# Optimization experiments

Hardware: AMD Instinct MI355X
Metric: run time of the kernel (lower is better)

## Reference

```python
import jax, jax.numpy as jnp
import numpy as np

B_, N_, D_ = 8, 1024, 64
H_, DH_ = 4, 16
DI_, DS_, DTR_ = 128, 64, 4
MAXP = 512


def _ln(x, w, b, eps=1e-5):
    m = jnp.mean(x, -1, keepdims=True)
    v = jnp.mean((x - m) ** 2, -1, keepdims=True)
    return (x - m) * jax.lax.rsqrt(v + eps) * w + b


def _attn(x, drop_mask, Wq, Wkv, Wo, bo, rel_emb):
    b, n, d = x.shape
    scale = DH_ ** -0.5
    q = (x @ Wq).reshape(b, n, H_, DH_).transpose(0, 2, 1, 3)
    kv = x @ Wkv
    k = kv[..., :d].reshape(b, n, H_, DH_).transpose(0, 2, 1, 3)
    v = kv[..., d:].reshape(b, n, H_, DH_).transpose(0, 2, 1, 3)
    dots = jnp.einsum('bhid,bhjd->bhij', q, k) * scale
    seq = jnp.arange(n)
    dist = jnp.clip(seq[:, None] - seq[None, :], -MAXP, MAXP) + MAXP
    rpe = rel_emb[dist]  # (n, n, DH_)
    dots = dots + jnp.einsum('bhid,ijd->bhij', q, rpe) * scale
    # stochastic key drop: Bernoulli(0.3) positions get -1e12
    dots = dots + drop_mask.astype(dots.dtype) * (-1e12)
    attn = jax.nn.softmax(dots, axis=-1)
    out = jnp.einsum('bhij,bhjd->bhid', attn, v)
    out = out.transpose(0, 2, 1, 3).reshape(b, n, H_ * DH_)
    return out @ Wo + bo


def _mamba(x, W_in, conv_w, conv_b, W_xproj, W_dt, b_dt, A_log, Dm, W_out):
    b, n, _ = x.shape
    xz = x @ W_in                      # (b, n, 2*DI_)
    u, z = xz[..., :DI_], xz[..., DI_:]
    uc = u.transpose(0, 2, 1)          # (b, DI_, n)
    uc = jax.lax.conv_general_dilated(
        uc, conv_w[:, None, :], (1,), ((3, 0),),
        feature_group_count=DI_, dimension_numbers=('NCH', 'OIH', 'NCH'))
    uc = uc + conv_b[None, :, None]
    u = jax.nn.silu(uc).transpose(0, 2, 1)  # (b, n, DI_)
    xdb = u @ W_xproj                  # (b, n, DTR_+2*DS_)
    dt = jax.nn.softplus(xdb[..., :DTR_] @ W_dt + b_dt)  # (b, n, DI_)
    Bm = xdb[..., DTR_:DTR_ + DS_]
    Cm = xdb[..., DTR_ + DS_:]
    A = -jnp.exp(A_log)                # (DI_, DS_)

    def step(h, inp):
        dt_t, B_t, C_t, u_t = inp      # (b,DI_),(b,DS_),(b,DS_),(b,DI_)
        dA = jnp.exp(dt_t[..., None] * A)
        h = h * dA + (dt_t * u_t)[..., None] * B_t[:, None, :]
        y = jnp.einsum('bds,bs->bd', h, C_t)
        return h, y

    h0 = jnp.zeros((b, DI_, DS_), x.dtype)
    xs = (dt.transpose(1, 0, 2), Bm.transpose(1, 0, 2),
          Cm.transpose(1, 0, 2), u.transpose(1, 0, 2))
    _, ys = jax.lax.scan(step, h0, xs)
    y = ys.transpose(1, 0, 2) + u * Dm
    y = y * jax.nn.silu(z)
    return y @ W_out


def _rmsgn(x, gamma, eps=1e-5, groups=4):
    shp = x.shape
    dpg = shp[-1] // groups
    xg = x.reshape(shp[:-1] + (groups, dpg))
    rms = jnp.sqrt(jnp.sum(xg * xg, -1, keepdims=True)) * (dpg ** -0.5)
    return (xg / (rms + eps)).reshape(shp) * gamma


def _ff1(x, c1_w, c1_b, d1_w, d1_b):
    # SwiGLUConvDeconv1d(64, 256, kernel=4, shift=1); x: (b, s2, 64)
    s2 = x.shape[1]
    xc = x.transpose(0, 2, 1)
    xc = jnp.pad(xc, ((0, 0), (0, 0), (3, 3)))
    xc = jax.lax.conv_general_dilated(
        xc, c1_w, (1,), 'VALID', dimension_numbers=('NCH', 'OIH', 'NCH'))
    xc = xc + c1_b[None, :, None]
    gate = jax.nn.silu(xc[:, 256:, :])
    xc = xc[:, :256, :] * gate
    # ConvTranspose1d stride 1 == conv with flipped kernel, full padding
    w = jnp.flip(d1_w, -1).transpose(1, 0, 2)  # (64, 256, 4)
    xc = jax.lax.conv_general_dilated(
        xc, w, (1,), ((3, 3),), dimension_numbers=('NCH', 'OIH', 'NCH'))
    xc = xc + d1_b[None, :, None]
    out = xc.transpose(0, 2, 1)
    return out[:, 3:3 + s2, :]


def _forward(x, drop_mask, ln1_w, ln1_b, Wq, Wkv, Wo, bo, rel_emb,
             ln2_w, ln2_b, W_in, conv_w, conv_b, W_xproj, W_dt, b_dt,
             A_log, Dm, W_out, gamma, c1_w, c1_b, d1_w, d1_b, ln3_w, ln3_b):
    xt = _ln(x, ln1_w, ln1_b)
    xt = _attn(xt, drop_mask, Wq, Wkv, Wo, bo, rel_emb) + x
    x = x + xt  # dropout p=0 -> identity (faithful to original residual math)
    xt = _ln(x, ln2_w, ln2_b)
    m = _mamba(xt, W_in, conv_w, conv_b, W_xproj, W_dt, b_dt, A_log, Dm, W_out)
    m = jnp.where(m >= 0, m, 0.01 * m)  # leaky_relu
    m = _rmsgn(m, gamma)
    m = m + 0.5 * _ff1(m, c1_w, c1_b, d1_w, d1_b)
    x = x + m
    return _ln(x, ln3_w, ln3_b)


def setup_inputs() -> dict:
    ks = jax.random.split(jax.random.key(0), 16)
    g = lambda i, shp, s: jax.random.normal(ks[i], shp, dtype=jnp.float32) * s
    A_log = jnp.log(jnp.tile(jnp.arange(1, DS_ + 1, dtype=jnp.float32)[None, :], (DI_, 1)))
    return {
        'x': jax.random.normal(ks[0], (B_, N_, D_), dtype=jnp.float32),
        'drop_mask': jax.random.bernoulli(ks[1], 0.3, (B_, H_, N_, N_)),
        'ln1_w': jnp.ones((D_,), jnp.float32), 'ln1_b': jnp.zeros((D_,), jnp.float32),
        'Wq': g(2, (D_, D_), 0.1), 'Wkv': g(3, (D_, 2 * D_), 0.1),
        'Wo': g(4, (D_, D_), 0.1), 'bo': jnp.zeros((D_,), jnp.float32),
        'rel_emb': g(5, (2 * MAXP + 1, DH_), 0.02),
        'ln2_w': jnp.ones((D_,), jnp.float32), 'ln2_b': jnp.zeros((D_,), jnp.float32),
        'W_in': g(6, (D_, 2 * DI_), 0.1),
        'conv_w': g(7, (DI_, 4), 0.2), 'conv_b': jnp.zeros((DI_,), jnp.float32),
        'W_xproj': g(8, (DI_, DTR_ + 2 * DS_), 0.1),
        'W_dt': g(9, (DTR_, DI_), 0.1), 'b_dt': jnp.zeros((DI_,), jnp.float32),
        'A_log': A_log, 'Dm': jnp.ones((DI_,), jnp.float32),
        'W_out': g(10, (DI_, D_), 0.1),
        'gamma': jnp.ones((D_,), jnp.float32),
        'c1_w': g(11, (512, 64, 4), 0.1), 'c1_b': jnp.zeros((512,), jnp.float32),
        'd1_w': g(12, (256, 64, 4), 0.1), 'd1_b': jnp.zeros((64,), jnp.float32),
        'ln3_w': jnp.ones((D_,), jnp.float32), 'ln3_b': jnp.zeros((D_,), jnp.float32),
    }


def reference(x, drop_mask, ln1_w, ln1_b, Wq, Wkv, Wo, bo, rel_emb,
              ln2_w, ln2_b, W_in, conv_w, conv_b, W_xproj, W_dt, b_dt,
              A_log, Dm, W_out, gamma, c1_w, c1_b, d1_w, d1_b, ln3_w, ln3_b):
    return _forward(x, drop_mask, ln1_w, ln1_b, Wq, Wkv, Wo, bo, rel_emb,
                    ln2_w, ln2_b, W_in, conv_w, conv_b, W_xproj, W_dt, b_dt,
                    A_log, Dm, W_out, gamma, c1_w, c1_b, d1_w, d1_b, ln3_w, ln3_b)
```

## Files before the change

kernel.cpp:

```cpp
#include <hip/hip_runtime.h>
#include <math.h>


__device__ __forceinline__ float wsum64(float v){
#pragma unroll
  for(int m=32;m>0;m>>=1) v += __shfl_xor(v, m, 64);
  return v;
}
__device__ __forceinline__ float wmax64(float v){
#pragma unroll
  for(int m=32;m>0;m>>=1) v = fmaxf(v, __shfl_xor(v, m, 64));
  return v;
}
__device__ __forceinline__ float silu_f(float x){ return x / (1.f + __expf(-x)); }
__device__ __forceinline__ int clip512(int d){ return d < -512 ? -512 : (d > 512 ? 512 : d); }

__global__ __launch_bounds__(256) void k_ln1_qkv(
    const float* __restrict__ x, const float* __restrict__ w1, const float* __restrict__ b1,
    const float* __restrict__ Wq, const float* __restrict__ Wkv,
    const float* __restrict__ rel, const float* __restrict__ c1w,
    float* __restrict__ qb, float2* __restrict__ kvT4,
    float* __restrict__ relT, float* __restrict__ c1wT){
  int lane = threadIdx.x & 63, warp = threadIdx.x >> 6;
  int token = blockIdx.x*4 + warp;
  __shared__ float xt[4][64];
  float xv = x[(size_t)token*64 + lane];
  float mean = wsum64(xv) * 0.015625f;
  float dlt = xv - mean;
  float var = wsum64(dlt*dlt) * 0.015625f;
  float xn = dlt * rsqrtf(var + 1e-5f) * w1[lane] + b1[lane];
  xt[warp][lane] = xn;
  __syncthreads();
  float aq=0.f, ak=0.f, av=0.f;
#pragma unroll 4
  for(int dd=0; dd<64; ++dd){
    float xd = xt[warp][dd];
    aq += xd * Wq[dd*64 + lane];
    ak += xd * Wkv[dd*128 + lane];
    av += xd * Wkv[dd*128 + 64 + lane];
  }
  int b = token >> 10, i = token & 1023;
  int h = lane >> 4, dh = lane & 15;
  size_t o  = (((size_t)(b*4 + h))*1024 + i)*16 + dh;
  qb[o]=aq;
  int c2 = dh >> 1, half = dh & 1;
  size_t o2 = ((((size_t)(b*4 + h))*8 + c2)*1024 + i)*2 + half;
  kvT4[o2] = make_float2(ak, av);

  if (blockIdx.x < 65){
    int idx = blockIdx.x*256 + threadIdx.x;
    if (idx < 16*1025){
      int c = idx / 1025;
      int d = idx - c*1025;
      relT[idx] = rel[d*16 + c];
    }
  } else if (blockIdx.x < 577){
    int idx = (blockIdx.x-65)*256 + threadIdx.x;
    int row = idx >> 9;
    int ii  = idx & 511;
    c1wT[idx] = c1w[(size_t)ii*256 + row];
  }
}

__global__ __launch_bounds__(256) void k_kmax(
    const float4* __restrict__ kvT4, float* __restrict__ Kmax){
  int bh = blockIdx.x; int tid = threadIdx.x;
  const float4* base = kvT4 + (size_t)bh*8*1024;
  float mx = 0.f;
#pragma unroll
  for(int r=0;r<4;++r){
    int j = tid + 256*r;
    float ss = 0.f;
#pragma unroll
    for(int c2=0;c2<8;++c2){ float4 kv = base[c2*1024 + j]; ss += kv.x*kv.x + kv.z*kv.z; }
    mx = fmaxf(mx, ss);
  }
  mx = wmax64(mx);
  __shared__ float red[4];
  int lane = tid&63, wv = tid>>6;
  if(lane==0) red[wv]=mx;
  __syncthreads();
  if(tid==0) Kmax[bh] = sqrtf(fmaxf(fmaxf(red[0],red[1]),fmaxf(red[2],red[3])));
}

__global__ __launch_bounds__(256, 4) void k_attn(
    const float* __restrict__ qb, const float4* __restrict__ kvT4,
    const int* __restrict__ dmask, const float* __restrict__ relT,
    const float* __restrict__ Kmax, float* __restrict__ attn_raw){
  int tid = threadIdx.x;
  int lane = tid & 63, wv = tid >> 6;
  int bh  = blockIdx.y;
  int i0  = blockIdx.x*8;
  int b = bh >> 2, h = bh & 3;
  int r0 = wv*2, r1 = wv*2 + 1;

  __shared__ float Gc[8][1024];
  __shared__ float qs[8][16];
  __shared__ float gmS[8];
  __shared__ float Ms[8];
  __shared__ float sums[8];

  if (tid < 128){
    int r = tid >> 4, c = tid & 15;
    qs[r][c] = qb[((size_t)bh*1024 + i0 + r)*16 + c] * 0.25f;
  }
  __syncthreads();

  {
    int r = tid >> 5, jb = tid & 31;
    float qr[16];
#pragma unroll
    for(int c=0;c<16;++c) qr[c] = qs[r][c];
    float gmax = -3.0e38f;
#pragma unroll 1
    for(int k=0;k<32;++k){
      int j = jb + 32*k;
      int d = clip512(i0 + r - j) + 512;
      float g = 0.f;
#pragma unroll
      for(int c=0;c<16;++c) g += qr[c]*relT[c*1025 + d];
      Gc[r][j] = g;
      gmax = fmaxf(gmax, g);
    }
#pragma unroll
    for(int m=1;m<32;m<<=1) gmax = fmaxf(gmax, __shfl_xor(gmax, m, 64));
    if ((lane&31)==0) gmS[r] = gmax;
  }
  __syncthreads();
  if (tid < 8){
    float qn = 0.f;
#pragma unroll
    for(int c=0;c<16;++c) qn += qs[tid][c]*qs[tid][c];
    Ms[tid] = gmS[tid] + sqrtf(qn)*Kmax[bh];
  }
  __syncthreads();

  float q0[16], q1[16];
#pragma unroll
  for(int c=0;c<16;++c){ q0[c]=qs[r0][c]; q1[c]=qs[r1][c]; }
  float M0 = Ms[r0], M1 = Ms[r1];

  const float4* kvb = kvT4 + (size_t)bh*8*1024;
  const int* mb0 = dmask + ((size_t)bh*1024 + i0 + r0)*1024;
  const int* mb1 = dmask + ((size_t)bh*1024 + i0 + r1)*1024;

  float s0=0.f, s1=0.f;
  float a0[16], a1[16];
#pragma unroll
  for(int c=0;c<16;++c){ a0[c]=0.f; a1[c]=0.f; }

#pragma unroll 1
  for(int t=0;t<16;++t){
    int j = lane + 64*t;
    int mk0 = mb0[j], mk1 = mb1[j];
    float4 kv[8];
#pragma unroll
    for(int c2=0;c2<8;++c2) kv[c2] = kvb[c2*1024 + j];
    float sv0 = Gc[r0][j], sv1 = Gc[r1][j];
#pragma unroll
    for(int c2=0;c2<8;++c2){
      sv0 += q0[2*c2]*kv[c2].x + q0[2*c2+1]*kv[c2].z;
      sv1 += q1[2*c2]*kv[c2].x + q1[2*c2+1]*kv[c2].z;
    }
    float p0 = mk0 ? 0.f : __expf(sv0 - M0);
    float p1 = mk1 ? 0.f : __expf(sv1 - M1);
    s0 += p0; s1 += p1;
#pragma unroll
    for(int c2=0;c2<8;++c2){
      a0[2*c2]   += p0*kv[c2].y; a0[2*c2+1] += p0*kv[c2].w;
      a1[2*c2]   += p1*kv[c2].y; a1[2*c2+1] += p1*kv[c2].w;
    }
  }
  s0 = wsum64(s0); s1 = wsum64(s1);
#pragma unroll
  for(int c=0;c<16;++c){
    float x0 = a0[c];
    x0 += __shfl_xor(x0, 32, 64); x0 += __shfl_xor(x0, 16, 64);
    a0[c] = x0;
    float x1 = a1[c];
    x1 += __shfl_xor(x1, 32, 64); x1 += __shfl_xor(x1, 16, 64);
    a1[c] = x1;
  }
  __syncthreads();
  float* red = &Gc[0][0];
  if (lane < 16){
#pragma unroll
    for(int c=0;c<16;++c){
      red[r0*272 + lane*17 + c] = a0[c];
      red[r1*272 + lane*17 + c] = a1[c];
    }
  }
  if (lane == 0){ sums[r0] = s0; sums[r1] = s1; }
  __syncthreads();
  if (tid < 128){
    int row = tid >> 4, c = tid & 15;
    float tot = 0.f;
#pragma unroll
    for(int g=0; g<16; ++g) tot += red[row*272 + g*17 + c];
    attn_raw[((size_t)b*1024 + i0 + row)*64 + h*16 + c] = tot / sums[row];
  }
}

__global__ __launch_bounds__(256) void k_post_attn(
    const float* __restrict__ x, const float* __restrict__ attn_raw,
    const float* __restrict__ Wo, const float* __restrict__ bo,
    const float* __restrict__ ln2w, const float* __restrict__ ln2b,
    const float* __restrict__ W_in,
    float* __restrict__ x2, float* __restrict__ u0, float* __restrict__ zsarr){
  int lane = threadIdx.x & 63, warp = threadIdx.x >> 6;
  int token = blockIdx.x*4 + warp;
  __shared__ float ar[4][64];
  __shared__ float lnv[4][64];
  ar[warp][lane] = attn_raw[(size_t)token*64 + lane];
  __syncthreads();
  float acc = bo[lane];
#pragma unroll 4
  for(int dd=0;dd<64;++dd) acc += ar[warp][dd]*Wo[dd*64+lane];
  float t = 2.f*x[(size_t)token*64+lane] + acc;
  x2[(size_t)token*64+lane] = t;
  float mean = wsum64(t)*0.015625f;
  float dlt = t-mean;
  float var = wsum64(dlt*dlt)*0.015625f;
  float ln = dlt*rsqrtf(var+1e-5f)*ln2w[lane]+ln2b[lane];
  lnv[warp][lane]=ln;
  __syncthreads();
  float a0=0.f,a1=0.f,a2=0.f,a3=0.f;
#pragma unroll 4
  for(int dd=0;dd<64;++dd){
    float xd = lnv[warp][dd];
    const float* wr = W_in + dd*256;
    a0 += xd*wr[lane]; a1 += xd*wr[lane+64]; a2 += xd*wr[lane+128]; a3 += xd*wr[lane+192];
  }
  u0[(size_t)token*128 + lane] = a0;
  u0[(size_t)token*128 + 64 + lane] = a1;
  zsarr[(size_t)token*128 + lane] = silu_f(a2);
  zsarr[(size_t)token*128 + 64 + lane] = silu_f(a3);
}

__global__ __launch_bounds__(256) void k_conv_proj(
    const float* __restrict__ u0, const float* __restrict__ conv_w, const float* __restrict__ conv_b,
    const float* __restrict__ W_xproj, const float* __restrict__ W_dt, const float* __restrict__ b_dt,
    float* __restrict__ uarr, float* __restrict__ Bmp, float* __restrict__ Cmp, float* __restrict__ dtarr){
  int sub = threadIdx.x >> 7, c = threadIdx.x & 127;
  int token = blockIdx.x*2 + sub;
  int b = token >> 10, i = token & 1023;
  __shared__ float us[2][128];
  __shared__ float dtin[2][4];
  float acc = conv_b[c];
#pragma unroll
  for(int k2=0;k2<4;++k2){
    int t2 = i - 3 + k2;
    if (t2 >= 0) acc += u0[((size_t)b*1024 + t2)*128 + c]*conv_w[c*4+k2];
  }
  float uv = silu_f(acc);
  uarr[(size_t)token*128 + c] = uv;
  us[sub][c] = uv;
  __syncthreads();
  float accA = 0.f, accB = 0.f;
  int cB = 128 + (c & 3);
#pragma unroll 4
  for(int dd=0; dd<128; ++dd){
    float xd = us[sub][dd];
    accA += xd * W_xproj[dd*132 + c];
    accB += xd * W_xproj[dd*132 + cB];
  }
  if (c < 4){ dtin[sub][c] = accA; Cmp[(size_t)token*64 + 60 + c] = accB; }
  else if (c < 68) Bmp[(size_t)token*64 + (c-4)] = accA;
  else             Cmp[(size_t)token*64 + (c-68)] = accA;
  __syncthreads();
  float dv = b_dt[c];
#pragma unroll
  for(int r2=0;r2<4;++r2) dv += dtin[sub][r2]*W_dt[r2*128 + c];
  dv = fmaxf(dv, 0.f) + log1pf(expf(-fabsf(dv)));
  dtarr[(size_t)token*128 + c] = dv;
}

__global__ __launch_bounds__(256) void k_scan_a(
    const float* __restrict__ dtarr, const float* __restrict__ uarr,
    const float* __restrict__ Bmp, const float* __restrict__ A_log,
    float* __restrict__ Parr, float* __restrict__ Rarr){
  int lane = threadIdx.x & 63, warp = threadIdx.x >> 6;
  int w = blockIdx.x*4 + warp;
  int c = w & 7, d = (w >> 3) & 127, b = w >> 10;
  float A = -expf(A_log[d*64 + lane]);
  int tb = c*128;
  const float* dtp = dtarr + ((size_t)b*1024 + tb)*128 + d;
  const float* up  = uarr  + ((size_t)b*1024 + tb)*128 + d;
  const float* Bp  = Bmp   + ((size_t)b*1024 + tb)*64 + lane;
  float R = 0.f, sdt = 0.f;
  for(int t0=0; t0<128; t0+=8){
    float dtc[8], uc[8], Bc[8];
#pragma unroll
    for(int r=0;r<8;++r){
      dtc[r]=dtp[(size_t)(t0+r)*128]; uc[r]=up[(size_t)(t0+r)*128]; Bc[r]=Bp[(size_t)(t0+r)*64];
    }
#pragma unroll
    for(int r=0;r<8;++r){
      float dt = dtc[r];
      R = R*__expf(dt*A) + dt*uc[r]*Bc[r];
      sdt += dt;
    }
  }
  Parr[(size_t)w*64 + lane] = __expf(sdt*A);
  Rarr[(size_t)w*64 + lane] = R;
}

__global__ __launch_bounds__(256) void k_scan_c(
    const float* __restrict__ dtarr, const float* __restrict__ uarr,
    const float* __restrict__ Bmp, const float* __restrict__ Cmp,
    const float* __restrict__ zsarr, const float* __restrict__ A_log,
    const float* __restrict__ Dm, const float* __restrict__ Parr,
    const float* __restrict__ Rarr, float* __restrict__ ymp){
  int lane = threadIdx.x & 63, warp = threadIdx.x >> 6;
  int w = blockIdx.x*4 + warp;
  int c = w & 7, d = (w >> 3) & 127, b = w >> 10;
  float A = -expf(A_log[d*64 + lane]);
  float Dv = Dm[d];
  float h = 0.f;
  int wbase = w - c;
#pragma unroll 1
  for(int cp=0; cp<c; ++cp){
    float P = Parr[(size_t)(wbase+cp)*64 + lane];
    float R = Rarr[(size_t)(wbase+cp)*64 + lane];
    h = h*P + R;
  }
  int tb = c*128;
  const float* dtp = dtarr + ((size_t)b*1024 + tb)*128 + d;
  const float* up  = uarr  + ((size_t)b*1024 + tb)*128 + d;
  const float* zp  = zsarr + ((size_t)b*1024 + tb)*128 + d;
  const float* Bp  = Bmp   + ((size_t)b*1024 + tb)*64 + lane;
  const float* Cp  = Cmp   + ((size_t)b*1024 + tb)*64 + lane;
  float* yp        = ymp   + ((size_t)b*1024 + tb)*128 + d;
  for(int t0=0; t0<128; t0+=8){
    float dtc[8], uc[8], Bc[8], Cc[8], zc[8];
#pragma unroll
    for(int r=0;r<8;++r){
      dtc[r]=dtp[(size_t)(t0+r)*128]; uc[r]=up[(size_t)(t0+r)*128];
      Bc[r]=Bp[(size_t)(t0+r)*64];    Cc[r]=Cp[(size_t)(t0+r)*64];
      zc[r]=zp[(size_t)(t0+r)*128];
    }
    float hc[8];
#pragma unroll
    for(int r=0;r<8;++r){
      float dt = dtc[r];
      h = h*__expf(dt*A) + dt*uc[r]*Bc[r];
      hc[r] = h*Cc[r];
    }
    float y[8];
#pragma unroll
    for(int r=0;r<8;++r) y[r] = wsum64(hc[r]);
    if (lane==0){
#pragma unroll
      for(int r=0;r<8;++r) yp[(size_t)(t0+r)*128] = (y[r] + uc[r]*Dv)*zc[r];
    }
  }
}

__global__ __launch_bounds__(256) void k_wout(
    const float* __restrict__ ymp, const float* __restrict__ W_out,
    const float* __restrict__ gamma, float* __restrict__ marr){
  int lane = threadIdx.x & 63, warp = threadIdx.x >> 6;
  int token = blockIdx.x*4 + warp;
  __shared__ float ys[4][128];
  ys[warp][lane]      = ymp[(size_t)token*128 + lane];
  ys[warp][lane+64]   = ymp[(size_t)token*128 + 64 + lane];
  __syncthreads();
  float acc = 0.f;
#pragma unroll 4
  for(int dd=0; dd<128; ++dd) acc += ys[warp][dd]*W_out[dd*64 + lane];
  acc = acc >= 0.f ? acc : 0.01f*acc;
  float ss = acc*acc;
#pragma unroll
  for(int m=1;m<16;m<<=1) ss += __shfl_xor(ss, m, 64);
  float rms = sqrtf(ss)*0.25f;
  marr[(size_t)token*64 + lane] = acc/(rms + 1e-5f)*gamma[lane];
}

__global__ __launch_bounds__(256) void k_h2(
    const float* __restrict__ marr, const float* __restrict__ c1wT,
    const float* __restrict__ c1b, float* __restrict__ h2){
  int b = blockIdx.y;
  int t0 = blockIdx.x * 16;
  int tid = threadIdx.x;
  __shared__ float ms[19][64];
  for(int l = tid; l < 19*64; l += 256){
    int row = l >> 6, cc = l & 63;
    int t = t0 - 3 + row;
    ms[row][cc] = (t >= 0 && t < 1024) ? marr[((size_t)b*1024 + t)*64 + cc] : 0.f;
  }
  __syncthreads();
  int i = tid;
  float acc1[16], acc2[16];
#pragma unroll
  for(int tl=0;tl<16;++tl){ acc1[tl]=0.f; acc2[tl]=0.f; }
  for(int cc=0; cc<64; ++cc){
    float mv[19];
#pragma unroll
    for(int r2=0;r2<19;++r2) mv[r2] = ms[r2][cc];
    const float* wr = c1wT + (size_t)cc*4*512;
    float wa0 = wr[      i], wa1 = wr[ 512+i], wa2 = wr[1024+i], wa3 = wr[1536+i];
    float wg0 = wr[  256+i], wg1 = wr[ 768+i], wg2 = wr[1280+i], wg3 = wr[1792+i];
#pragma unroll
    for(int tl=0; tl<16; ++tl){
      acc1[tl] += wa0*mv[tl+0] + wa1*mv[tl+1] + wa2*mv[tl+2] + wa3*mv[tl+3];
      acc2[tl] += wg0*mv[tl+0] + wg1*mv[tl+1] + wg2*mv[tl+2] + wg3*mv[tl+3];
    }
  }
  float bb1 = c1b[i], bb2 = c1b[i+256];
#pragma unroll
  for(int tl=0; tl<16; ++tl){
    int t = t0 + tl;
    if (t < 1027){
      float o1 = acc1[tl] + bb1;
      float o2 = acc2[tl] + bb2;
      h2[((size_t)b*1027 + t)*256 + i] = o1 * silu_f(o2);
    }
  }
}

__global__ __launch_bounds__(256) void k_ff_final(
    const float* __restrict__ h2, const float* __restrict__ d1w, const float* __restrict__ d1b,
    const float* __restrict__ x2, const float* __restrict__ marr,
    const float* __restrict__ ln3w, const float* __restrict__ ln3b,
    float* __restrict__ out){
  int b = blockIdx.y;
  int s0 = blockIdx.x * 16;
  int tid = threadIdx.x;
  int o = tid & 63, sg = tid >> 6;
  __shared__ float hs[19][256];
  for(int l = tid; l < 19*256; l += 256){
    int row = l >> 8, cc = l & 255;
    hs[row][cc] = h2[((size_t)b*1027 + s0 + row)*256 + cc];
  }
  __syncthreads();
  int sl = sg*4;
  float acc0=0.f, acc1=0.f, acc2=0.f, acc3=0.f;
  const float4* wb = (const float4*)d1w + o;
#pragma unroll 2
  for(int i2=0; i2<256; ++i2){
    float4 wv = wb[(size_t)i2*64];
    float h0=hs[sl+0][i2], h1=hs[sl+1][i2], h2v=hs[sl+2][i2], h3=hs[sl+3][i2];
    float h4=hs[sl+4][i2], h5=hs[sl+5][i2], h6=hs[sl+6][i2];
    acc0 += h0*wv.w + h1*wv.z + h2v*wv.y + h3*wv.x;
    acc1 += h1*wv.w + h2v*wv.z + h3*wv.y + h4*wv.x;
    acc2 += h2v*wv.w + h3*wv.z + h4*wv.y + h5*wv.x;
    acc3 += h3*wv.w + h4*wv.z + h5*wv.y + h6*wv.x;
  }
  float accs[4] = {acc0, acc1, acc2, acc3};
  float bo_ = d1b[o];
#pragma unroll
  for(int r=0;r<4;++r){
    int s = s0 + sl + r;
    size_t idx = ((size_t)b*1024 + s)*64 + o;
    float tot = x2[idx] + marr[idx] + 0.5f*(accs[r] + bo_);
    float mean = wsum64(tot)*0.015625f;
    float dlt = tot - mean;
    float var = wsum64(dlt*dlt)*0.015625f;
    out[idx] = dlt*rsqrtf(var+1e-5f)*ln3w[o] + ln3b[o];
  }
}

extern "C" void kernel_launch(void* const* d_in, const int* in_sizes, int n_in,
                              void* d_out, int out_size, void* d_ws, size_t ws_size,
                              hipStream_t stream){
  const float* x       = (const float*)d_in[0];
  const int*   dmask   = (const int*)  d_in[1];
  const float* ln1w    = (const float*)d_in[2];
  const float* ln1b    = (const float*)d_in[3];
  const float* Wq      = (const float*)d_in[4];
  const float* Wkv     = (const float*)d_in[5];
  const float* Wo      = (const float*)d_in[6];
  const float* bo      = (const float*)d_in[7];
  const float* rel     = (const float*)d_in[8];
  const float* ln2w    = (const float*)d_in[9];
  const float* ln2b    = (const float*)d_in[10];
  const float* W_in    = (const float*)d_in[11];
  const float* conv_w  = (const float*)d_in[12];
  const float* conv_b  = (const float*)d_in[13];
  const float* W_xproj = (const float*)d_in[14];
  const float* W_dt    = (const float*)d_in[15];
  const float* b_dt    = (const float*)d_in[16];
  const float* A_log   = (const float*)d_in[17];
  const float* Dm      = (const float*)d_in[18];
  const float* W_out   = (const float*)d_in[19];
  const float* gamma   = (const float*)d_in[20];
  const float* c1w     = (const float*)d_in[21];
  const float* c1b     = (const float*)d_in[22];
  const float* d1w     = (const float*)d_in[23];
  const float* d1b     = (const float*)d_in[24];
  const float* ln3w    = (const float*)d_in[25];
  const float* ln3b    = (const float*)d_in[26];
  float* outp = (float*)d_out;

  float* ws = (float*)d_ws;
  float* qb       = ws;
  float* kvT4     = qb      + 524288;
  float* attn_raw = kvT4    + 1048576;
  float* x2       = attn_raw+ 524288;
  float* u0       = x2      + 524288;
  float* zsarr    = u0      + 1048576;
  float* uarr     = zsarr   + 1048576;
  float* dtarr    = uarr    + 1048576;
  float* Bmp      = dtarr   + 1048576;
  float* Cmp      = Bmp     + 524288;
  float* ymp      = Cmp     + 524288;
  float* marr     = ymp     + 1048576;
  float* h2       = marr    + 524288;
  float* relT     = h2      + 2103296;
  float* c1wT     = relT    + 16400;
  float* Parr     = c1wT    + 131072;
  float* Rarr     = Parr    + 524288;
  float* Kmaxa    = Rarr    + 524288;

  k_ln1_qkv  <<<2048, 256, 0, stream>>>(x, ln1w, ln1b, Wq, Wkv, rel, c1w,
                                        qb, (float2*)kvT4, relT, c1wT);
  k_kmax     <<<32, 256, 0, stream>>>((const float4*)kvT4, Kmaxa);
  k_attn     <<<dim3(128,32), 256, 0, stream>>>(qb, (const float4*)kvT4, dmask, relT, Kmaxa, attn_raw);
  k_post_attn<<<2048, 256, 0, stream>>>(x, attn_raw, Wo, bo, ln2w, ln2b, W_in, x2, u0, zsarr);
  k_conv_proj<<<4096, 256, 0, stream>>>(u0, conv_w, conv_b, W_xproj, W_dt, b_dt, uarr, Bmp, Cmp, dtarr);
  k_scan_a   <<<2048, 256, 0, stream>>>(dtarr, uarr, Bmp, A_log, Parr, Rarr);
  k_scan_c   <<<2048, 256, 0, stream>>>(dtarr, uarr, Bmp, Cmp, zsarr, A_log, Dm, Parr, Rarr, ymp);
  k_wout     <<<2048, 256, 0, stream>>>(ymp, W_out, gamma, marr);
  k_h2       <<<dim3(65,8), 256, 0, stream>>>(marr, c1wT, c1b, h2);
  k_ff_final <<<dim3(64,8), 256, 0, stream>>>(h2, d1w, d1b, x2, marr, ln3w, ln3b, outp);
}
```

Baseline: 814.1 us.

## Compute relative-position bias per distance once per block and use float2 KV layout

The attention kernel now computes the q·rel_emb bias once for each distinct distance value (1025 per 8-row tile) and scatters it into the Gc tile. Clipped regions are filled from the two boundary values, replacing 8192 per-element 16-wide dot products with gathered relT reads. The K/V buffer changes from float4 pairs to a float2 per head-dimension layout, so the main loop issues 16 float2 loads instead of 8 float4 loads. The occupancy hint on k_attn drops from 4 to 3 blocks per SM, which allows more registers but risks less latency hiding.

```diff
diff --git a/kernel.cpp b/kernel.cpp
--- a/kernel.cpp
+++ b/kernel.cpp
@@ -13,13 +13,12 @@
   return v;
 }
 __device__ __forceinline__ float silu_f(float x){ return x / (1.f + __expf(-x)); }
-__device__ __forceinline__ int clip512(int d){ return d < -512 ? -512 : (d > 512 ? 512 : d); }
 
 __global__ __launch_bounds__(256) void k_ln1_qkv(
     const float* __restrict__ x, const float* __restrict__ w1, const float* __restrict__ b1,
     const float* __restrict__ Wq, const float* __restrict__ Wkv,
     const float* __restrict__ rel, const float* __restrict__ c1w,
-    float* __restrict__ qb, float2* __restrict__ kvT4,
+    float* __restrict__ qb, float2* __restrict__ kvT,
     float* __restrict__ relT, float* __restrict__ c1wT){
   int lane = threadIdx.x & 63, warp = threadIdx.x >> 6;
   int token = blockIdx.x*4 + warp;
@@ -42,10 +41,9 @@
   int b = token >> 10, i = token & 1023;
   int h = lane >> 4, dh = lane & 15;
   size_t o  = (((size_t)(b*4 + h))*1024 + i)*16 + dh;
+  size_t oT = (((size_t)(b*4 + h))*16 + dh)*1024 + i;
   qb[o]=aq;
-  int c2 = dh >> 1, half = dh & 1;
-  size_t o2 = ((((size_t)(b*4 + h))*8 + c2)*1024 + i)*2 + half;
-  kvT4[o2] = make_float2(ak, av);
+  kvT[oT] = make_float2(ak, av);
 
   if (blockIdx.x < 65){
     int idx = blockIdx.x*256 + threadIdx.x;
@@ -63,16 +61,16 @@
 }
 
 __global__ __launch_bounds__(256) void k_kmax(
-    const float4* __restrict__ kvT4, float* __restrict__ Kmax){
+    const float2* __restrict__ kvT, float* __restrict__ Kmax){
   int bh = blockIdx.x; int tid = threadIdx.x;
-  const float4* base = kvT4 + (size_t)bh*8*1024;
+  const float2* base = kvT + (size_t)bh*16*1024;
   float mx = 0.f;
 #pragma unroll
   for(int r=0;r<4;++r){
     int j = tid + 256*r;
     float ss = 0.f;
 #pragma unroll
-    for(int c2=0;c2<8;++c2){ float4 kv = base[c2*1024 + j]; ss += kv.x*kv.x + kv.z*kv.z; }
+    for(int c=0;c<16;++c){ float2 kv = base[c*1024 + j]; ss += kv.x*kv.x; }
     mx = fmaxf(mx, ss);
   }
   mx = wmax64(mx);
@@ -83,8 +81,8 @@
   if(tid==0) Kmax[bh] = sqrtf(fmaxf(fmaxf(red[0],red[1]),fmaxf(red[2],red[3])));
 }
 
-__global__ __launch_bounds__(256, 4) void k_attn(
-    const float* __restrict__ qb, const float4* __restrict__ kvT4,
+__global__ __launch_bounds__(256, 3) void k_attn(
+    const float* __restrict__ qb, const float2* __restrict__ kvT,
     const int* __restrict__ dmask, const float* __restrict__ relT,
     const float* __restrict__ Kmax, float* __restrict__ attn_raw){
   int tid = threadIdx.x;
@@ -96,6 +94,7 @@
 
   __shared__ float Gc[8][1024];
   __shared__ float qs[8][16];
+  __shared__ float G0s[8], G1024s[8];
   __shared__ float gmS[8];
   __shared__ float Ms[8];
   __shared__ float sums[8];
@@ -106,25 +105,49 @@
   }
   __syncthreads();
 
+#pragma unroll 1
+  for(int bb=0; bb<5; ++bb){
+    int d = tid + 256*bb;
+    if (d <= 1024){
+      float rl[16];
+#pragma unroll
+      for(int c=0;c<16;++c) rl[c] = relT[c*1025 + d];
+#pragma unroll
+      for(int r=0;r<8;++r){
+        float g = 0.f;
+#pragma unroll
+        for(int c=0;c<16;++c) g += qs[r][c]*rl[c];
+        if (d == 0)        G0s[r] = g;
+        else if (d == 1024) G1024s[r] = g;
+        else {
+          int j = i0 + r + 512 - d;
+          if (j >= 0 && j < 1024) Gc[r][j] = g;
+        }
+      }
+    }
+  }
+  __syncthreads();
+#pragma unroll
+  for(int r=0;r<8;++r){
+    float g0 = G0s[r], g1 = G1024s[r];
+    int lo = i0 + r - 512;
+    int hi = i0 + r + 512;
+#pragma unroll
+    for(int p=0;p<4;++p){
+      int j = tid + 256*p;
+      if (j >= hi) Gc[r][j] = g0;
+      else if (j <= lo) Gc[r][j] = g1;
+    }
+  }
+  __syncthreads();
   {
     int r = tid >> 5, jb = tid & 31;
-    float qr[16];
-#pragma unroll
-    for(int c=0;c<16;++c) qr[c] = qs[r][c];
-    float gmax = -3.0e38f;
-#pragma unroll 1
-    for(int k=0;k<32;++k){
-      int j = jb + 32*k;
-      int d = clip512(i0 + r - j) + 512;
-      float g = 0.f;
-#pragma unroll
-      for(int c=0;c<16;++c) g += qr[c]*relT[c*1025 + d];
-      Gc[r][j] = g;
-      gmax = fmaxf(gmax, g);
-    }
-#pragma unroll
-    for(int m=1;m<32;m<<=1) gmax = fmaxf(gmax, __shfl_xor(gmax, m, 64));
-    if ((lane&31)==0) gmS[r] = gmax;
+    float gm = -3.0e38f;
+#pragma unroll
+    for(int k=0;k<32;++k) gm = fmaxf(gm, Gc[r][jb + 32*k]);
+#pragma unroll
+    for(int m=1;m<32;m<<=1) gm = fmaxf(gm, __shfl_xor(gm, m, 64));
+    if ((lane&31)==0) gmS[r] = gm;
   }
   __syncthreads();
   if (tid < 8){
@@ -140,7 +163,7 @@
   for(int c=0;c<16;++c){ q0[c]=qs[r0][c]; q1[c]=qs[r1][c]; }
   float M0 = Ms[r0], M1 = Ms[r1];
 
-  const float4* kvb = kvT4 + (size_t)bh*8*1024;
+  const float2* kvb = kvT + (size_t)bh*16*1024;
   const int* mb0 = dmask + ((size_t)bh*1024 + i0 + r0)*1024;
   const int* mb1 = dmask + ((size_t)bh*1024 + i0 + r1)*1024;
 
@@ -153,23 +176,17 @@
   for(int t=0;t<16;++t){
     int j = lane + 64*t;
     int mk0 = mb0[j], mk1 = mb1[j];
-    float4 kv[8];
-#pragma unroll
-    for(int c2=0;c2<8;++c2) kv[c2] = kvb[c2*1024 + j];
+    float2 kv[16];
+#pragma unroll
+    for(int c=0;c<16;++c) kv[c] = kvb[c*1024 + j];
     float sv0 = Gc[r0][j], sv1 = Gc[r1][j];
 #pragma unroll
-    for(int c2=0;c2<8;++c2){
-      sv0 += q0[2*c2]*kv[c2].x + q0[2*c2+1]*kv[c2].z;
-      sv1 += q1[2*c2]*kv[c2].x + q1[2*c2+1]*kv[c2].z;
-    }
+    for(int c=0;c<16;++c){ sv0 += q0[c]*kv[c].x; sv1 += q1[c]*kv[c].x; }
     float p0 = mk0 ? 0.f : __expf(sv0 - M0);
     float p1 = mk1 ? 0.f : __expf(sv1 - M1);
     s0 += p0; s1 += p1;
 #pragma unroll
-    for(int c2=0;c2<8;++c2){
-      a0[2*c2]   += p0*kv[c2].y; a0[2*c2+1] += p0*kv[c2].w;
-      a1[2*c2]   += p1*kv[c2].y; a1[2*c2+1] += p1*kv[c2].w;
-    }
+    for(int c=0;c<16;++c){ a0[c] += p0*kv[c].y; a1[c] += p1*kv[c].y; }
   }
   s0 = wsum64(s0); s1 = wsum64(s1);
 #pragma unroll
@@ -494,8 +511,8 @@
 
   float* ws = (float*)d_ws;
   float* qb       = ws;
-  float* kvT4     = qb      + 524288;
-  float* attn_raw = kvT4    + 1048576;
+  float* kvT      = qb      + 524288;
+  float* attn_raw = kvT     + 1048576;
   float* x2       = attn_raw+ 524288;
   float* u0       = x2      + 524288;
   float* zsarr    = u0      + 1048576;
@@ -513,9 +530,9 @@
   float* Kmaxa    = Rarr    + 524288;
 
   k_ln1_qkv  <<<2048, 256, 0, stream>>>(x, ln1w, ln1b, Wq, Wkv, rel, c1w,
-                                        qb, (float2*)kvT4, relT, c1wT);
-  k_kmax     <<<32, 256, 0, stream>>>((const float4*)kvT4, Kmaxa);
-  k_attn     <<<dim3(128,32), 256, 0, stream>>>(qb, (const float4*)kvT4, dmask, relT, Kmaxa, attn_raw);
+                                        qb, (float2*)kvT, relT, c1wT);
+  k_kmax     <<<32, 256, 0, stream>>>((const float2*)kvT, Kmaxa);
+  k_attn     <<<dim3(128,32), 256, 0, stream>>>(qb, (const float2*)kvT, dmask, relT, Kmaxa, attn_raw);
   k_post_attn<<<2048, 256, 0, stream>>>(x, attn_raw, Wo, bo, ln2w, ln2b, W_in, x2, u0, zsarr);
   k_conv_proj<<<4096, 256, 0, stream>>>(u0, conv_w, conv_b, W_xproj, W_dt, b_dt, uarr, Bmp, Cmp, dtarr);
   k_scan_a   <<<2048, 256, 0, stream>>>(dtarr, uarr, Bmp, A_log, Parr, Rarr);
```

Result: faster. 738.4 us (-9.3%).
